# Kernel optimization log

Measured on AMD Instinct MI355X. Metric: run time of the kernel, lower is better.

The kernel has to match this reference:

```python
import jax, jax.numpy as jnp
import numpy as np

NUM_USER = 100000
NUM_ITEM = 50000
N_NODES = NUM_USER + NUM_ITEM
N_EDGES = 4800000
DIM = 64
N_LAYERS = 4


def setup_inputs() -> dict:
    key = jax.random.key(0)
    k1, k2, k3, k4, k5 = jax.random.split(key, 5)
    user_emb = jax.random.normal(k1, (NUM_USER, DIM), dtype=jnp.float32)
    item_emb = jax.random.normal(k2, (NUM_ITEM, DIM), dtype=jnp.float32)
    edge_val = jax.random.uniform(k3, (N_EDGES,), dtype=jnp.float32)
    edge_row = jax.random.randint(k4, (N_EDGES,), 0, N_NODES, dtype=jnp.int32)
    edge_col = jax.random.randint(k5, (N_EDGES,), 0, N_NODES, dtype=jnp.int32)
    return {
        "user_emb": user_emb,
        "item_emb": item_emb,
        "edge_val": edge_val,
        "edge_row": edge_row,
        "edge_col": edge_col,
    }


def _spmm(edge_val, edge_row, edge_col, x):
    # out[r] = sum_{e: row[e]==r} val[e] * x[col[e]]  -- COO SpMM
    msgs = edge_val[:, None] * x[edge_col]  # [E, D]
    return jax.ops.segment_sum(msgs, edge_row, num_segments=N_NODES)


def reference(user_emb, item_emb, edge_val, edge_row, edge_col):
    # LightGCN.forward: concat embeddings, 4 spmm propagation layers,
    # return last layer split into user/item parts.
    x = jnp.concatenate([user_emb, item_emb], axis=0)  # [N, 64]
    for _ in range(N_LAYERS):
        x = _spmm(edge_val, edge_row, edge_col, x)
    return x[:NUM_USER], x[NUM_USER:]
```

## Files before the change

### kernel.cpp

```cpp
#include <hip/hip_runtime.h>

#define DIM 64
#define BSH 8
#define BROWS 256
#define MAXNB 1023
#define EPB 8192
#define MAXNBLK 1024

__global__ void zero_f4(float* __restrict__ p, size_t n4) {
    size_t i = (size_t)blockIdx.x * blockDim.x + threadIdx.x;
    size_t stride = (size_t)gridDim.x * blockDim.x;
    float4 z = make_float4(0.f, 0.f, 0.f, 0.f);
    for (; i < n4; i += stride)
        reinterpret_cast<float4*>(p)[i] = z;
}

__device__ __forceinline__ unsigned int bf16_rne(float f) {
    unsigned int u = __float_as_uint(f);
    return (u + 0x7FFFu + ((u >> 16) & 1u)) >> 16;
}

__global__ void f32_to_bf16(const float* __restrict__ src,
                            unsigned short* __restrict__ dst, int n4) {
    int i = blockIdx.x * blockDim.x + threadIdx.x;
    int stride = gridDim.x * blockDim.x;
    for (; i < n4; i += stride) {
        float4 v = *reinterpret_cast<const float4*>(src + (size_t)i * 4);
        ushort4 o;
        o.x = (unsigned short)bf16_rne(v.x);
        o.y = (unsigned short)bf16_rne(v.y);
        o.z = (unsigned short)bf16_rne(v.z);
        o.w = (unsigned short)bf16_rne(v.w);
        *reinterpret_cast<ushort4*>(dst + (size_t)i * 4) = o;
    }
}

__global__ __launch_bounds__(1024) void count_chunks(const int* __restrict__ row,
                                                     int* __restrict__ runcnt,
                                                     int ne, int nb) {
    __shared__ int h[1024];
    int blk = blockIdx.x, t = threadIdx.x;
    h[t] = 0;
    __syncthreads();
    int base = blk * EPB;
    int lim = base + EPB; if (lim > ne) lim = ne;
    for (int e = base + t; e < lim; e += 1024)
        atomicAdd(&h[row[e] >> BSH], 1);
    __syncthreads();
    if (t < nb) runcnt[(size_t)blk * nb + t] = h[t];
}

__global__ __launch_bounds__(1024) void scan_chunks(int* __restrict__ runcnt,
                                                    int* __restrict__ btotal,
                                                    int nb, int nblk) {
    __shared__ int sc[1024];
    int b = blockIdx.x, t = threadIdx.x;
    int v = (t < nblk) ? runcnt[(size_t)t * nb + b] : 0;
    sc[t] = v;
    __syncthreads();
    for (int d = 1; d < 1024; d <<= 1) {
        int a = (t >= d) ? sc[t - d] : 0;
        __syncthreads();
        sc[t] += a;
        __syncthreads();
    }
    if (t < nblk) runcnt[(size_t)t * nb + b] = sc[t] - v;
    if (t == 1023) btotal[b] = sc[1023];
}

__global__ __launch_bounds__(1024) void scan_buckets(const int* __restrict__ btotal,
                                                     int* __restrict__ bstart, int nb) {
    __shared__ int sc[1024];
    int t = threadIdx.x;
    int v = (t < nb) ? btotal[t] : 0;
    sc[t] = v;
    __syncthreads();
    for (int d = 1; d < 1024; d <<= 1) {
        int a = (t >= d) ? sc[t - d] : 0;
        __syncthreads();
        sc[t] += a;
        __syncthreads();
    }
    if (t < nb) bstart[t] = sc[t] - v;
    if (t == 0) bstart[nb] = sc[1023];
}

__global__ __launch_bounds__(1024) void scatter2(const int* __restrict__ row,
                                                 const int* __restrict__ col,
                                                 const float* __restrict__ val,
                                                 const int* __restrict__ bstart,
                                                 const int* __restrict__ runcnt,
                                                 int2* __restrict__ ebuf,
                                                 int ne, int nb) {
    __shared__ int cur[1024];
    int blk = blockIdx.x, t = threadIdx.x;
    if (t < nb) cur[t] = bstart[t] + runcnt[(size_t)blk * nb + t];
    __syncthreads();
    int base = blk * EPB;
    int lim = base + EPB; if (lim > ne) lim = ne;
    for (int e = base + t; e < lim; e += 1024) {
        int r = row[e];
        int pos = atomicAdd(&cur[r >> BSH], 1);
        ebuf[pos] = make_int2(col[e] | ((r & (BROWS - 1)) << 18), __float_as_int(val[e]));
    }
}

__global__ __launch_bounds__(512) void local_sort(const int2* __restrict__ ein,
                                                  const int* __restrict__ bstart,
                                                  int2* __restrict__ eout,
                                                  int* __restrict__ rowptr,
                                                  int nrows, int nb) {
    __shared__ int hist[BROWS];
    __shared__ int cur[BROWS];
    __shared__ int wsum[4];
    int b = blockIdx.x;
    int t = threadIdx.x;
    int beg = bstart[b], end = bstart[b + 1];
    if (t < BROWS) hist[t] = 0;
    __syncthreads();
    for (int e = beg + t; e < end; e += 512)
        atomicAdd(&hist[((unsigned)ein[e].x) >> 18], 1);
    __syncthreads();
    int v = 0, s = 0;
    if (t < BROWS) {
        v = hist[t];
        s = v;
        #pragma unroll
        for (int off = 1; off < 64; off <<= 1) {
            int a = __shfl_up(s, off);
            if ((t & 63) >= off) s += a;
        }
        if ((t & 63) == 63) wsum[t >> 6] = s;
    }
    __syncthreads();
    if (t < BROWS) {
        int woff = 0;
        #pragma unroll
        for (int w = 0; w < 4; ++w)
            if (w < (t >> 6)) woff += wsum[w];
        int excl = woff + s - v;
        cur[t] = excl;
        int r = (b << BSH) + t;
        if (r < nrows) rowptr[r] = beg + excl;
    }
    if (b == nb - 1 && t == 0) rowptr[nrows] = end;
    __syncthreads();
    for (int e = beg + t; e < end; e += 512) {
        int2 cv = ein[e];
        int rl = ((unsigned)cv.x) >> 18;
        int pos = beg + atomicAdd(&cur[rl], 1);
        eout[pos] = make_int2(cv.x & 0x3FFFF, cv.y);
    }
}

template<bool OUT16>
__global__ __launch_bounds__(256) void spmm_bf16(const int2* __restrict__ colval,
                                                 const int* __restrict__ rowptr,
                                                 const unsigned short* __restrict__ xb,
                                                 float* __restrict__ yf,
                                                 unsigned short* __restrict__ yb,
                                                 int nrows) {
    int wid  = (int)(((size_t)blockIdx.x * blockDim.x + threadIdx.x) >> 6);
    int lane = threadIdx.x & 63;
    if (wid >= nrows) return;
    int sub = lane >> 3;
    int q8  = (lane & 7) << 3;

    int beg = rowptr[wid];
    int end = rowptr[wid + 1];
    int len = end - beg;
    int nfull = len >> 3;

    float acc[8];
    #pragma unroll
    for (int k = 0; k < 8; ++k) acc[k] = 0.f;

    int e = beg + sub;
    #pragma unroll 4
    for (int g = 0; g < nfull; ++g, e += 8) {
        int2 cv = colval[e];
        float v = __int_as_float(cv.y);
        uint4 x = *reinterpret_cast<const uint4*>(xb + (size_t)cv.x * DIM + q8);
        acc[0] = fmaf(v, __uint_as_float(x.x << 16),          acc[0]);
        acc[1] = fmaf(v, __uint_as_float(x.x & 0xffff0000u),  acc[1]);
        acc[2] = fmaf(v, __uint_as_float(x.y << 16),          acc[2]);
        acc[3] = fmaf(v, __uint_as_float(x.y & 0xffff0000u),  acc[3]);
        acc[4] = fmaf(v, __uint_as_float(x.z << 16),          acc[4]);
        acc[5] = fmaf(v, __uint_as_float(x.z & 0xffff0000u),  acc[5]);
        acc[6] = fmaf(v, __uint_as_float(x.w << 16),          acc[6]);
        acc[7] = fmaf(v, __uint_as_float(x.w & 0xffff0000u),  acc[7]);
    }
    int rem = len & 7;
    if (sub < rem) {
        int2 cv = colval[e];
        float v = __int_as_float(cv.y);
        uint4 x = *reinterpret_cast<const uint4*>(xb + (size_t)cv.x * DIM + q8);
        acc[0] = fmaf(v, __uint_as_float(x.x << 16),          acc[0]);
        acc[1] = fmaf(v, __uint_as_float(x.x & 0xffff0000u),  acc[1]);
        acc[2] = fmaf(v, __uint_as_float(x.y << 16),          acc[2]);
        acc[3] = fmaf(v, __uint_as_float(x.y & 0xffff0000u),  acc[3]);
        acc[4] = fmaf(v, __uint_as_float(x.z << 16),          acc[4]);
        acc[5] = fmaf(v, __uint_as_float(x.z & 0xffff0000u),  acc[5]);
        acc[6] = fmaf(v, __uint_as_float(x.w << 16),          acc[6]);
        acc[7] = fmaf(v, __uint_as_float(x.w & 0xffff0000u),  acc[7]);
    }

    #pragma unroll
    for (int off = 8; off <= 32; off <<= 1) {
        #pragma unroll
        for (int k = 0; k < 8; ++k)
            acc[k] += __shfl_xor(acc[k], off);
    }

    if (sub == 0) {
        if (OUT16) {
            uint4 o;
            o.x = bf16_rne(acc[0]) | (bf16_rne(acc[1]) << 16);
            o.y = bf16_rne(acc[2]) | (bf16_rne(acc[3]) << 16);
            o.z = bf16_rne(acc[4]) | (bf16_rne(acc[5]) << 16);
            o.w = bf16_rne(acc[6]) | (bf16_rne(acc[7]) << 16);
            *reinterpret_cast<uint4*>(yb + (size_t)wid * DIM + q8) = o;
        } else {
            float* dst = yf + (size_t)wid * DIM + q8;
            *reinterpret_cast<float4*>(dst)     = make_float4(acc[0], acc[1], acc[2], acc[3]);
            *reinterpret_cast<float4*>(dst + 4) = make_float4(acc[4], acc[5], acc[6], acc[7]);
        }
    }
}

__global__ void spmm_atomic(const float* __restrict__ val,
                            const int* __restrict__ row,
                            const int* __restrict__ col,
                            const float* __restrict__ p0,
                            const float* __restrict__ p1,
                            int split,
                            float* __restrict__ y,
                            int nedges) {
    long long t = (long long)blockIdx.x * blockDim.x + threadIdx.x;
    int e = (int)(t >> 4);
    if (e >= nedges) return;
    int d = ((int)t & 15) << 2;
    float v = val[e];
    int r = row[e];
    int c = col[e];
    const float* src = (c < split) ? (p0 + (size_t)c * DIM)
                                   : (p1 + (size_t)(c - split) * DIM);
    float4 xv = *reinterpret_cast<const float4*>(src + d);
    float* o = y + (size_t)r * DIM + d;
    unsafeAtomicAdd(o + 0, v * xv.x);
    unsafeAtomicAdd(o + 1, v * xv.y);
    unsafeAtomicAdd(o + 2, v * xv.z);
    unsafeAtomicAdd(o + 3, v * xv.w);
}

extern "C" void kernel_launch(void* const* d_in, const int* in_sizes, int n_in,
                              void* d_out, int out_size, void* d_ws, size_t ws_size,
                              hipStream_t stream) {
    const float* user = (const float*)d_in[0];
    const float* item = (const float*)d_in[1];
    const float* val  = (const float*)d_in[2];
    const int*   row  = (const int*)d_in[3];
    const int*   col  = (const int*)d_in[4];

    int nU = in_sizes[0] / DIM;
    int nI = in_sizes[1] / DIM;
    int nE = in_sizes[2];
    int nN = nU + nI;
    int nb = (nN + BROWS - 1) >> BSH;
    int nblk = (nE + EPB - 1) / EPB;
    size_t bufElems = (size_t)nN * DIM;
    size_t n4 = bufElems / 4;

    char* base = (char*)d_ws;
    size_t off = 0;
    auto alloc = [&](size_t bytes) -> void* {
        void* p = base + off;
        off = (off + bytes + 255) & ~(size_t)255;
        return p;
    };
    size_t xBytes = bufElems * sizeof(float);
    size_t eBytes = (size_t)nE * sizeof(int2);
    size_t bBytes = bufElems * 2 * sizeof(unsigned short);
    size_t r0 = xBytes > eBytes ? xBytes : eBytes;
    if (bBytes > r0) r0 = bBytes;
    char*  region0 = (char*)alloc(r0);
    int2*  colval  = (int2*)alloc(eBytes);
    int*   rowptr  = (int*)alloc((size_t)(nN + 1) * sizeof(int));
    int*   runcnt  = (int*)alloc((size_t)nblk * nb * sizeof(int));
    int*   btotal  = (int*)alloc((size_t)nb * sizeof(int));
    int*   bstart  = (int*)alloc((size_t)(nb + 1) * sizeof(int));
    size_t needed  = off;

    float* Y = (float*)d_out;

    if (ws_size >= needed && nb <= MAXNB && nblk <= MAXNBLK && nN < (1 << 18)) {
        int2* ebuf = (int2*)region0;
        unsigned short* B0 = (unsigned short*)region0;
        unsigned short* B1 = B0 + bufElems;

        count_chunks<<<nblk, 1024, 0, stream>>>(row, runcnt, nE, nb);
        scan_chunks<<<nb, 1024, 0, stream>>>(runcnt, btotal, nb, nblk);
        scan_buckets<<<1, 1024, 0, stream>>>(btotal, bstart, nb);
        scatter2<<<nblk, 1024, 0, stream>>>(row, col, val, bstart, runcnt, ebuf, nE, nb);
        local_sort<<<nb, 512, 0, stream>>>(ebuf, bstart, colval, rowptr, nN, nb);

        int cu = (nU * DIM) / 4, ci = (nI * DIM) / 4;
        f32_to_bf16<<<2048, 256, 0, stream>>>(user, B0, cu);
        f32_to_bf16<<<2048, 256, 0, stream>>>(item, B0 + (size_t)nU * DIM, ci);

        int sgrid = (int)(((size_t)nN * 64 + 255) / 256);
        spmm_bf16<true ><<<sgrid, 256, 0, stream>>>(colval, rowptr, B0, nullptr, B1, nN);
        spmm_bf16<true ><<<sgrid, 256, 0, stream>>>(colval, rowptr, B1, nullptr, B0, nN);
        spmm_bf16<true ><<<sgrid, 256, 0, stream>>>(colval, rowptr, B0, nullptr, B1, nN);
        spmm_bf16<false><<<sgrid, 256, 0, stream>>>(colval, rowptr, B1, Y, nullptr, nN);
    } else {
        float* X = (float*)region0;
        int zblocks = (int)((n4 + 255) / 256);
        if (zblocks > 4096) zblocks = 4096;
        long long totalThreads = (long long)nE * 16;
        dim3 sgrid((unsigned)((totalThreads + 255) / 256));
        const float* Xu = X;
        const float* Xi = X + (size_t)nU * DIM;
        const float* Yu = Y;
        const float* Yi = Y + (size_t)nU * DIM;
        zero_f4<<<zblocks, 256, 0, stream>>>(X, n4);
        spmm_atomic<<<sgrid, 256, 0, stream>>>(val, row, col, user, item, nU, X, nE);
        zero_f4<<<zblocks, 256, 0, stream>>>(Y, n4);
        spmm_atomic<<<sgrid, 256, 0, stream>>>(val, row, col, Xu, Xi, nU, Y, nE);
        zero_f4<<<zblocks, 256, 0, stream>>>(X, n4);
        spmm_atomic<<<sgrid, 256, 0, stream>>>(val, row, col, Yu, Yi, nU, X, nE);
        zero_f4<<<zblocks, 256, 0, stream>>>(Y, n4);
        spmm_atomic<<<sgrid, 256, 0, stream>>>(val, row, col, Xu, Xi, nU, Y, nE);
    }
}
```

Baseline: 459.1 us.

## Stage bucket scatter in shared memory for coalesced global writes

The scatter kernel now first sorts each chunk's edges by bucket in LDS, using a local histogram and prefix scan, then writes them to global memory in bucket-contiguous runs instead of as random per-edge writes. The chunk size is halved to 4096 edges so the staging buffers fit in shared memory, and the chunk-scan kernel loops so it can handle more than 1024 chunks. This adds a second histogram pass and heavy LDS use per block, which may lower occupancy, in exchange for better write coalescing during the edge bucketing.

```diff
diff --git a/kernel.cpp b/kernel.cpp
--- a/kernel.cpp
+++ b/kernel.cpp
@@ -4,8 +4,8 @@
 #define BSH 8
 #define BROWS 256
 #define MAXNB 1023
-#define EPB 8192
-#define MAXNBLK 1024
+#define EPB 4096
+#define MAXNBLK 2048
 
 __global__ void zero_f4(float* __restrict__ p, size_t n4) {
     size_t i = (size_t)blockIdx.x * blockDim.x + threadIdx.x;
@@ -54,18 +54,28 @@
                                                     int* __restrict__ btotal,
                                                     int nb, int nblk) {
     __shared__ int sc[1024];
+    __shared__ int carry;
     int b = blockIdx.x, t = threadIdx.x;
-    int v = (t < nblk) ? runcnt[(size_t)t * nb + b] : 0;
-    sc[t] = v;
-    __syncthreads();
-    for (int d = 1; d < 1024; d <<= 1) {
-        int a = (t >= d) ? sc[t - d] : 0;
-        __syncthreads();
-        sc[t] += a;
-        __syncthreads();
-    }
-    if (t < nblk) runcnt[(size_t)t * nb + b] = sc[t] - v;
-    if (t == 1023) btotal[b] = sc[1023];
+    if (t == 0) carry = 0;
+    __syncthreads();
+    for (int off = 0; off < nblk; off += 1024) {
+        int i = off + t;
+        int v = (i < nblk) ? runcnt[(size_t)i * nb + b] : 0;
+        sc[t] = v;
+        __syncthreads();
+        for (int d = 1; d < 1024; d <<= 1) {
+            int a = (t >= d) ? sc[t - d] : 0;
+            __syncthreads();
+            sc[t] += a;
+            __syncthreads();
+        }
+        int excl = carry + sc[t] - v;
+        if (i < nblk) runcnt[(size_t)i * nb + b] = excl;
+        __syncthreads();
+        if (t == 1023) carry += sc[1023];
+        __syncthreads();
+    }
+    if (t == 0) btotal[b] = carry;
 }
 
 __global__ __launch_bounds__(1024) void scan_buckets(const int* __restrict__ btotal,
@@ -85,23 +95,55 @@
     if (t == 0) bstart[nb] = sc[1023];
 }
 
-__global__ __launch_bounds__(1024) void scatter2(const int* __restrict__ row,
+__global__ __launch_bounds__(1024) void scatter3(const int* __restrict__ row,
                                                  const int* __restrict__ col,
                                                  const float* __restrict__ val,
                                                  const int* __restrict__ bstart,
                                                  const int* __restrict__ runcnt,
                                                  int2* __restrict__ ebuf,
                                                  int ne, int nb) {
+    __shared__ int2 data[EPB];
+    __shared__ unsigned short bkt[EPB];
     __shared__ int cur[1024];
+    __shared__ int gbase[1024];
+    __shared__ int sc[1024];
     int blk = blockIdx.x, t = threadIdx.x;
-    if (t < nb) cur[t] = bstart[t] + runcnt[(size_t)blk * nb + t];
-    __syncthreads();
     int base = blk * EPB;
     int lim = base + EPB; if (lim > ne) lim = ne;
+    int len = lim - base;
+
+    cur[t] = 0;
+    __syncthreads();
+    for (int e = base + t; e < lim; e += 1024)
+        atomicAdd(&cur[row[e] >> BSH], 1);
+    __syncthreads();
+
+    int v = cur[t];
+    sc[t] = v;
+    __syncthreads();
+    for (int d = 1; d < 1024; d <<= 1) {
+        int a = (t >= d) ? sc[t - d] : 0;
+        __syncthreads();
+        sc[t] += a;
+        __syncthreads();
+    }
+    int excl = sc[t] - v;
+    if (t < nb) gbase[t] = bstart[t] + runcnt[(size_t)blk * nb + t] - excl;
+    cur[t] = excl;
+    __syncthreads();
+
     for (int e = base + t; e < lim; e += 1024) {
         int r = row[e];
-        int pos = atomicAdd(&cur[r >> BSH], 1);
-        ebuf[pos] = make_int2(col[e] | ((r & (BROWS - 1)) << 18), __float_as_int(val[e]));
+        int b = r >> BSH;
+        int pos = atomicAdd(&cur[b], 1);
+        data[pos] = make_int2(col[e] | ((r & (BROWS - 1)) << 18), __float_as_int(val[e]));
+        bkt[pos] = (unsigned short)b;
+    }
+    __syncthreads();
+
+    for (int i = t; i < len; i += 1024) {
+        int b = bkt[i];
+        ebuf[gbase[b] + i] = data[i];
     }
 }
 
@@ -301,7 +343,7 @@
         count_chunks<<<nblk, 1024, 0, stream>>>(row, runcnt, nE, nb);
         scan_chunks<<<nb, 1024, 0, stream>>>(runcnt, btotal, nb, nblk);
         scan_buckets<<<1, 1024, 0, stream>>>(btotal, bstart, nb);
-        scatter2<<<nblk, 1024, 0, stream>>>(row, col, val, bstart, runcnt, ebuf, nE, nb);
+        scatter3<<<nblk, 1024, 0, stream>>>(row, col, val, bstart, runcnt, ebuf, nE, nb);
         local_sort<<<nb, 512, 0, stream>>>(ebuf, bstart, colval, rowptr, nN, nb);
 
         int cu = (nU * DIM) / 4, ci = (nI * DIM) / 4;
```

New measurement: 445.8 us. 1.03x faster.
